# Kernel tuning notes

Hardware: AMD Instinct MI355X
Metric: run time of the kernel (lower is better)

The kernel has to match this reference:

```python
import jax, jax.numpy as jnp
import numpy as np

INPUTS, L1, L2, L3 = 40960, 256, 32, 32
B, K = 16384, 32  # batch, fixed active features per side


def setup_inputs() -> dict:
    key = jax.random.key(0)
    ks = jax.random.split(key, 12)
    wf = jax.random.randint(ks[0], (B * K,), 0, INPUTS, dtype=jnp.int64)
    bf = jax.random.randint(ks[1], (B * K,), 0, INPUTS, dtype=jnp.int64)
    offs = jnp.arange(B, dtype=jnp.int64) * K
    stm = jax.random.uniform(ks[2], (B,), dtype=jnp.float32)
    table = jax.random.normal(ks[3], (INPUTS, L1), dtype=jnp.float32) * 0.01
    ft_bias = jnp.zeros((L1,), dtype=jnp.float32)
    # xavier_uniform bounds: sqrt(6/(fan_in+fan_out))
    def xavier(k, shape):
        bound = np.sqrt(6.0 / (shape[0] + shape[1]))
        return jax.random.uniform(k, shape, jnp.float32, -bound, bound)
    W1 = xavier(ks[4], (L2, 2 * L1)); b1 = jnp.zeros((L2,), jnp.float32)
    W2 = xavier(ks[5], (L3, L2));     b2 = jnp.zeros((L3,), jnp.float32)
    Wo = xavier(ks[6], (1, L3));      bo = jnp.zeros((1,), jnp.float32)
    return {"white_features": wf, "white_offsets": offs, "black_features": bf,
            "black_offsets": offs, "stm": stm, "table": table, "ft_bias": ft_bias,
            "W1": W1, "b1": b1, "W2": W2, "b2": b2, "Wo": Wo, "bo": bo}


def _crelu(x):
    return jnp.clip(x, 0.0, 1.0)


def reference(white_features, white_offsets, black_features, black_offsets, stm,
              table, ft_bias, W1, b1, W2, b2, Wo, bo):
    nb = white_offsets.shape[0]
    # Uniform-bag EmbeddingBag(mode='sum'): gather rows and sum within each bag.
    w_acc = table[white_features.reshape(nb, -1)].sum(axis=1) + ft_bias  # [B, L1]
    b_acc = table[black_features.reshape(nb, -1)].sum(axis=1) + ft_bias  # [B, L1]
    wtm = jnp.concatenate([w_acc, b_acc], axis=1)  # [B, 2*L1]
    btm = jnp.concatenate([b_acc, w_acc], axis=1)
    s = stm.reshape(-1, 1)
    x = _crelu(s * wtm + (1.0 - s) * btm)
    x = _crelu(x @ W1.T + b1)
    x = _crelu(x @ W2.T + b2)
    return (x @ Wo.T + bo).squeeze(1)  # [B]
```

## Files before the change

kernel.cpp:

```cpp
#include <hip/hip_runtime.h>

#define KFEAT 32
#define NB 8
#define XPITCH 544
#define APITCH 272

__device__ __forceinline__ float clip01(float v) {
    return fminf(fmaxf(v, 0.0f), 1.0f);
}

__global__ __launch_bounds__(256) void quantize_table_i8(
    const float* __restrict__ src, uint* __restrict__ qt,
    float* __restrict__ scales, int nrows)
{
    const int row = blockIdx.x * 4 + (threadIdx.x >> 6);
    const int l   = threadIdx.x & 63;
    if (row >= nrows) return;

    const float4 v = reinterpret_cast<const float4*>(src)[(size_t)row * 64 + l];
    float m = fmaxf(fmaxf(fabsf(v.x), fabsf(v.y)), fmaxf(fabsf(v.z), fabsf(v.w)));
    m = fmaxf(m, __shfl_xor(m, 1));
    m = fmaxf(m, __shfl_xor(m, 2));
    m = fmaxf(m, __shfl_xor(m, 4));
    m = fmaxf(m, __shfl_xor(m, 8));
    m = fmaxf(m, __shfl_xor(m, 16));
    m = fmaxf(m, __shfl_xor(m, 32));

    const float inv = (m > 0.0f) ? 127.0f / m : 0.0f;
    const int b0 = ((int)rintf(v.x * inv)) & 0xFF;
    const int b1 = ((int)rintf(v.y * inv)) & 0xFF;
    const int b2 = ((int)rintf(v.z * inv)) & 0xFF;
    const int b3 = ((int)rintf(v.w * inv)) & 0xFF;
    qt[(size_t)row * 64 + l] = (uint)b0 | ((uint)b1 << 8) | ((uint)b2 << 16) | ((uint)b3 << 24);
    if (l == 0) scales[row] = m * (1.0f / 127.0f);
}

__global__ __launch_bounds__(256, 4) void nnue_i8_kernel(
    const int* __restrict__ wf, const int* __restrict__ bf,
    const float* __restrict__ stm, const uint* __restrict__ qt,
    const float* __restrict__ scales,
    const float* __restrict__ ft_bias,
    const float* __restrict__ W1, const float* __restrict__ b1,
    const float* __restrict__ W2, const float* __restrict__ b2,
    const float* __restrict__ Wo, const float* __restrict__ bo,
    float* __restrict__ out)
{
    __shared__ float lds[NB * XPITCH];
    __shared__ float y1s[NB][32];

    const int t   = threadIdx.x;
    const int l   = t & 63;
    const int w   = t >> 6;
    const int sub = l & 31;
    const int b0  = blockIdx.x * NB;

    {
        const int side = w & 1;
        const int eb   = w >> 1;
        const int* fp  = side ? bf : wf;

        #pragma unroll
        for (int g = 0; g < 4; ++g) {
            const int bag = g * 4 + w;
            const int iv  = fp[(size_t)(b0 + 2 * g + eb) * KFEAT + sub];

            uint v[KFEAT];
            #pragma unroll
            for (int k = 0; k < KFEAT; ++k) {
                const int row = __builtin_amdgcn_readlane(iv, k);
                v[k] = qt[(size_t)row * 64 + l];
            }

            float a0 = 0.f, a1 = 0.f, a2 = 0.f, a3 = 0.f;
            #pragma unroll
            for (int k = 0; k < KFEAT; ++k) {
                const int row  = __builtin_amdgcn_readlane(iv, k);
                const float sc = scales[row];
                const int  q   = (int)v[k];
                a0 = fmaf((float)((q << 24) >> 24), sc, a0);
                a1 = fmaf((float)((q << 16) >> 24), sc, a1);
                a2 = fmaf((float)((q <<  8) >> 24), sc, a2);
                a3 = fmaf((float)( q        >> 24), sc, a3);
            }
            *reinterpret_cast<float4*>(&lds[bag * APITCH + l * 4]) =
                make_float4(a0, a1, a2, a3);
        }
    }
    __syncthreads();

    {
        const int e = t >> 5, r = t & 31;
        const float s  = stm[b0 + e];
        const float os = 1.0f - s;
        const float4 wa0 = *reinterpret_cast<const float4*>(&lds[(2 * e + 0) * APITCH + 4 * r]);
        const float4 ba0 = *reinterpret_cast<const float4*>(&lds[(2 * e + 1) * APITCH + 4 * r]);
        const float4 wa1 = *reinterpret_cast<const float4*>(&lds[(2 * e + 0) * APITCH + 4 * (r + 32)]);
        const float4 ba1 = *reinterpret_cast<const float4*>(&lds[(2 * e + 1) * APITCH + 4 * (r + 32)]);
        const float4 fb0 = reinterpret_cast<const float4*>(ft_bias)[r];
        const float4 fb1 = reinterpret_cast<const float4*>(ft_bias)[r + 32];
        __syncthreads();

        #define MIXW(wa, ba, fb, i, hf)                                              \
        {                                                                            \
            float4 xv;                                                               \
            if (hf == 0) {                                                           \
                xv.x = clip01(fmaf(s, (wa).x, fmaf(os, (ba).x, (fb).x)));            \
                xv.y = clip01(fmaf(s, (wa).y, fmaf(os, (ba).y, (fb).y)));            \
                xv.z = clip01(fmaf(s, (wa).z, fmaf(os, (ba).z, (fb).z)));            \
                xv.w = clip01(fmaf(s, (wa).w, fmaf(os, (ba).w, (fb).w)));            \
            } else {                                                                 \
                xv.x = clip01(fmaf(s, (ba).x, fmaf(os, (wa).x, (fb).x)));            \
                xv.y = clip01(fmaf(s, (ba).y, fmaf(os, (wa).y, (fb).y)));            \
                xv.z = clip01(fmaf(s, (ba).z, fmaf(os, (wa).z, (fb).z)));            \
                xv.w = clip01(fmaf(s, (ba).w, fmaf(os, (wa).w, (fb).w)));            \
            }                                                                        \
            const int d = (hf) * 256 + 4 * (i);                                      \
            *reinterpret_cast<float4*>(&lds[e * XPITCH + (d >> 6) * 68 + (d & 63)]) = xv; \
        }
        MIXW(wa0, ba0, fb0, r,      0)
        MIXW(wa1, ba1, fb1, r + 32, 0)
        MIXW(wa0, ba0, fb0, r,      1)
        MIXW(wa1, ba1, fb1, r + 32, 1)
        #undef MIXW
    }
    __syncthreads();

    {
        const int j = t >> 3;
        const int c = t & 7;
        const float* w1p = W1 + j * 512 + c * 64;
        float acc[NB] = {0.f, 0.f, 0.f, 0.f, 0.f, 0.f, 0.f, 0.f};
        #pragma unroll
        for (int blk = 0; blk < 4; ++blk) {
            const float4 wv0 = reinterpret_cast<const float4*>(w1p + blk * 16)[0];
            const float4 wv1 = reinterpret_cast<const float4*>(w1p + blk * 16)[1];
            const float4 wv2 = reinterpret_cast<const float4*>(w1p + blk * 16)[2];
            const float4 wv3 = reinterpret_cast<const float4*>(w1p + blk * 16)[3];
            #pragma unroll
            for (int e = 0; e < NB; ++e) {
                const float* xp = &lds[e * XPITCH + c * 68 + blk * 16];
                const float4 x0 = *reinterpret_cast<const float4*>(xp + 0);
                const float4 x1 = *reinterpret_cast<const float4*>(xp + 4);
                const float4 x2 = *reinterpret_cast<const float4*>(xp + 8);
                const float4 x3 = *reinterpret_cast<const float4*>(xp + 12);
                float a = acc[e];
                a = fmaf(wv0.x, x0.x, a); a = fmaf(wv0.y, x0.y, a);
                a = fmaf(wv0.z, x0.z, a); a = fmaf(wv0.w, x0.w, a);
                a = fmaf(wv1.x, x1.x, a); a = fmaf(wv1.y, x1.y, a);
                a = fmaf(wv1.z, x1.z, a); a = fmaf(wv1.w, x1.w, a);
                a = fmaf(wv2.x, x2.x, a); a = fmaf(wv2.y, x2.y, a);
                a = fmaf(wv2.z, x2.z, a); a = fmaf(wv2.w, x2.w, a);
                a = fmaf(wv3.x, x3.x, a); a = fmaf(wv3.y, x3.y, a);
                a = fmaf(wv3.z, x3.z, a); a = fmaf(wv3.w, x3.w, a);
                acc[e] = a;
            }
        }
        #pragma unroll
        for (int e = 0; e < NB; ++e) {
            acc[e] += __shfl_xor(acc[e], 1);
            acc[e] += __shfl_xor(acc[e], 2);
            acc[e] += __shfl_xor(acc[e], 4);
        }
        if (c == 0) {
            const float bj = b1[j];
            #pragma unroll
            for (int e = 0; e < NB; ++e)
                y1s[e][j] = clip01(acc[e] + bj);
        }
    }
    __syncthreads();

    {
        const int e = t >> 5, i = t & 31;
        const float4* w2p = reinterpret_cast<const float4*>(W2 + i * 32);
        float a2 = b2[i];
        #pragma unroll
        for (int kq = 0; kq < 8; ++kq) {
            const float4 wq = w2p[kq];
            const float4 yq = *reinterpret_cast<const float4*>(&y1s[e][kq * 4]);
            a2 = fmaf(wq.x, yq.x, a2); a2 = fmaf(wq.y, yq.y, a2);
            a2 = fmaf(wq.z, yq.z, a2); a2 = fmaf(wq.w, yq.w, a2);
        }
        a2 = clip01(a2);
        float p = a2 * Wo[i];
        p += __shfl_xor(p, 1);  p += __shfl_xor(p, 2);
        p += __shfl_xor(p, 4);  p += __shfl_xor(p, 8);
        p += __shfl_xor(p, 16);
        if (i == 0) out[b0 + e] = p + bo[0];
    }
}

__global__ __launch_bounds__(256, 6) void nnue_fused_kernel(
    const int* __restrict__ wf, const int* __restrict__ bf,
    const float* __restrict__ stm, const float* __restrict__ table,
    const float* __restrict__ ft_bias,
    const float* __restrict__ W1, const float* __restrict__ b1,
    const float* __restrict__ W2, const float* __restrict__ b2,
    const float* __restrict__ Wo, const float* __restrict__ bo,
    float* __restrict__ out)
{
    __shared__ float4 accs[4][64];
    __shared__ float  xs[2 * 4 * 132];
    __shared__ float  y1s[2][32];

    const int t    = threadIdx.x;
    const int l    = t & 63;
    const int w    = t >> 6;
    const int side = w & 1;
    const int esub = w >> 1;

    const float4 ftb4 = reinterpret_cast<const float4*>(ft_bias)[l];
    const int*   fptr = side ? bf : wf;

    const int j = t >> 3;
    const int c = t & 7;
    const float* w1p = W1 + j * 512 + c * 64;
    const float* x0p = &xs[(0 * 4 + (c >> 1)) * 132 + (c & 1) * 64];
    const float* x1p = &xs[(1 * 4 + (c >> 1)) * 132 + (c & 1) * 64];

    for (int it = 0; it < 8 / 2; ++it) {
        const int b0 = blockIdx.x * 8 + it * 2;

        int idxv = fptr[(size_t)(b0 + esub) * KFEAT + (l & 31)];
        float4 acc = ftb4;
        #pragma unroll
        for (int k = 0; k < KFEAT; ++k) {
            const int row = __builtin_amdgcn_readlane(idxv, k);
            const float4 v = reinterpret_cast<const float4*>(table)[(size_t)row * 64 + l];
            acc.x += v.x; acc.y += v.y; acc.z += v.z; acc.w += v.w;
        }
        accs[w][l] = acc;
        __syncthreads();

        {
            const int e  = t >> 7;
            const int hf = (t >> 6) & 1;
            const int i  = t & 63;
            const float s  = stm[b0 + e];
            const float os = 1.0f - s;
            const float4 wa = accs[e * 2 + 0][i];
            const float4 ba = accs[e * 2 + 1][i];
            float4 x;
            if (hf == 0) {
                x.x = clip01(s * wa.x + os * ba.x);
                x.y = clip01(s * wa.y + os * ba.y);
                x.z = clip01(s * wa.z + os * ba.z);
                x.w = clip01(s * wa.w + os * ba.w);
            } else {
                x.x = clip01(s * ba.x + os * wa.x);
                x.y = clip01(s * ba.y + os * wa.y);
                x.z = clip01(s * ba.z + os * wa.z);
                x.w = clip01(s * ba.w + os * wa.w);
            }
            const int slot = hf * 64 + i;
            const int g = slot >> 5, i4 = slot & 31;
            *reinterpret_cast<float4*>(&xs[(e * 4 + g) * 132 + i4 * 4]) = x;
        }
        __syncthreads();

        float a0 = 0.0f, a1 = 0.0f;
        #pragma unroll 16
        for (int ii = 0; ii < 64; ++ii) {
            const float wv = w1p[ii];
            a0 = fmaf(wv, x0p[ii], a0);
            a1 = fmaf(wv, x1p[ii], a1);
        }
        a0 += __shfl_xor(a0, 1); a0 += __shfl_xor(a0, 2); a0 += __shfl_xor(a0, 4);
        a1 += __shfl_xor(a1, 1); a1 += __shfl_xor(a1, 2); a1 += __shfl_xor(a1, 4);
        if (c == 0) {
            const float bj = b1[j];
            y1s[0][j] = clip01(a0 + bj);
            y1s[1][j] = clip01(a1 + bj);
        }
        __syncthreads();

        if (t < 64) {
            const int e = t >> 5, i = t & 31;
            float a2 = b2[i];
            #pragma unroll
            for (int k2 = 0; k2 < 32; ++k2)
                a2 = fmaf(y1s[e][k2], W2[i * 32 + k2], a2);
            a2 = clip01(a2);
            float p = a2 * Wo[i];
            p += __shfl_xor(p, 1);  p += __shfl_xor(p, 2);
            p += __shfl_xor(p, 4);  p += __shfl_xor(p, 8);
            p += __shfl_xor(p, 16);
            if (i == 0) out[b0 + e] = p + bo[0];
        }
        __syncthreads();
    }
}

extern "C" void kernel_launch(void* const* d_in, const int* in_sizes, int n_in,
                              void* d_out, int out_size, void* d_ws, size_t ws_size,
                              hipStream_t stream) {
    const int*   wf      = (const int*)  d_in[0];
    const int*   bf      = (const int*)  d_in[2];
    const float* stm     = (const float*)d_in[4];
    const float* table   = (const float*)d_in[5];
    const float* ft_bias = (const float*)d_in[6];
    const float* W1      = (const float*)d_in[7];
    const float* b1      = (const float*)d_in[8];
    const float* W2      = (const float*)d_in[9];
    const float* b2      = (const float*)d_in[10];
    const float* Wo      = (const float*)d_in[11];
    const float* bo      = (const float*)d_in[12];
    float*       out     = (float*)d_out;

    const int B = in_sizes[1];
    const int tbl_elems = in_sizes[5];
    const int nrows = tbl_elems / 256;
    const size_t qbytes = (size_t)tbl_elems;
    const size_t need = qbytes + (size_t)nrows * sizeof(float);

    if (ws_size >= need) {
        uint*  qt     = (uint*)d_ws;
        float* scales = (float*)((char*)d_ws + qbytes);
        quantize_table_i8<<<(nrows + 3) / 4, 256, 0, stream>>>(table, qt, scales, nrows);
        nnue_i8_kernel<<<B / NB, 256, 0, stream>>>(
            wf, bf, stm, qt, scales, ft_bias, W1, b1, W2, b2, Wo, bo, out);
    } else {
        nnue_fused_kernel<<<B / 8, 256, 0, stream>>>(
            wf, bf, stm, table, ft_bias, W1, b1, W2, b2, Wo, bo, out);
    }
}
```

Before: 61.79 us.

## Retile L1 matvec to 4 outputs per thread group and fuse gather loads

```diff
diff --git a/kernel.cpp b/kernel.cpp
--- a/kernel.cpp
+++ b/kernel.cpp
@@ -63,20 +63,12 @@
         for (int g = 0; g < 4; ++g) {
             const int bag = g * 4 + w;
             const int iv  = fp[(size_t)(b0 + 2 * g + eb) * KFEAT + sub];
-
-            uint v[KFEAT];
-            #pragma unroll
-            for (int k = 0; k < KFEAT; ++k) {
-                const int row = __builtin_amdgcn_readlane(iv, k);
-                v[k] = qt[(size_t)row * 64 + l];
-            }
-
             float a0 = 0.f, a1 = 0.f, a2 = 0.f, a3 = 0.f;
             #pragma unroll
             for (int k = 0; k < KFEAT; ++k) {
                 const int row  = __builtin_amdgcn_readlane(iv, k);
+                const int  q   = (int)qt[(size_t)row * 64 + l];
                 const float sc = scales[row];
-                const int  q   = (int)v[k];
                 a0 = fmaf((float)((q << 24) >> 24), sc, a0);
                 a1 = fmaf((float)((q << 16) >> 24), sc, a1);
                 a2 = fmaf((float)((q <<  8) >> 24), sc, a2);
@@ -126,46 +118,75 @@
     __syncthreads();
 
     {
-        const int j = t >> 3;
-        const int c = t & 7;
-        const float* w1p = W1 + j * 512 + c * 64;
-        float acc[NB] = {0.f, 0.f, 0.f, 0.f, 0.f, 0.f, 0.f, 0.f};
-        #pragma unroll
-        for (int blk = 0; blk < 4; ++blk) {
-            const float4 wv0 = reinterpret_cast<const float4*>(w1p + blk * 16)[0];
-            const float4 wv1 = reinterpret_cast<const float4*>(w1p + blk * 16)[1];
-            const float4 wv2 = reinterpret_cast<const float4*>(w1p + blk * 16)[2];
-            const float4 wv3 = reinterpret_cast<const float4*>(w1p + blk * 16)[3];
-            #pragma unroll
-            for (int e = 0; e < NB; ++e) {
-                const float* xp = &lds[e * XPITCH + c * 68 + blk * 16];
+        const int jg = t >> 5;
+        const int ch = t & 31;
+        const float* w1p = W1 + (4 * jg) * 512 + ch * 16;
+
+        float4 wreg[4][4];
+        #pragma unroll
+        for (int r = 0; r < 4; ++r)
+            #pragma unroll
+            for (int q = 0; q < 4; ++q)
+                wreg[r][q] = *reinterpret_cast<const float4*>(w1p + r * 512 + q * 4);
+
+        const float4 b14 = *reinterpret_cast<const float4*>(b1 + 4 * jg);
+        const int d = ch * 16;
+        const int xoff = (d >> 6) * 68 + (d & 63);
+
+        #pragma unroll
+        for (int eh = 0; eh < 2; ++eh) {
+            float acc[4][4];
+            #pragma unroll
+            for (int r = 0; r < 4; ++r)
+                #pragma unroll
+                for (int el = 0; el < 4; ++el) acc[r][el] = 0.0f;
+
+            #pragma unroll
+            for (int el = 0; el < 4; ++el) {
+                const int e = eh * 4 + el;
+                const float* xp = &lds[e * XPITCH + xoff];
                 const float4 x0 = *reinterpret_cast<const float4*>(xp + 0);
                 const float4 x1 = *reinterpret_cast<const float4*>(xp + 4);
                 const float4 x2 = *reinterpret_cast<const float4*>(xp + 8);
                 const float4 x3 = *reinterpret_cast<const float4*>(xp + 12);
-                float a = acc[e];
-                a = fmaf(wv0.x, x0.x, a); a = fmaf(wv0.y, x0.y, a);
-                a = fmaf(wv0.z, x0.z, a); a = fmaf(wv0.w, x0.w, a);
-                a = fmaf(wv1.x, x1.x, a); a = fmaf(wv1.y, x1.y, a);
-                a = fmaf(wv1.z, x1.z, a); a = fmaf(wv1.w, x1.w, a);
-                a = fmaf(wv2.x, x2.x, a); a = fmaf(wv2.y, x2.y, a);
-                a = fmaf(wv2.z, x2.z, a); a = fmaf(wv2.w, x2.w, a);
-                a = fmaf(wv3.x, x3.x, a); a = fmaf(wv3.y, x3.y, a);
-                a = fmaf(wv3.z, x3.z, a); a = fmaf(wv3.w, x3.w, a);
-                acc[e] = a;
+                #pragma unroll
+                for (int r = 0; r < 4; ++r) {
+                    float a = acc[r][el];
+                    a = fmaf(wreg[r][0].x, x0.x, a); a = fmaf(wreg[r][0].y, x0.y, a);
+                    a = fmaf(wreg[r][0].z, x0.z, a); a = fmaf(wreg[r][0].w, x0.w, a);
+                    a = fmaf(wreg[r][1].x, x1.x, a); a = fmaf(wreg[r][1].y, x1.y, a);
+                    a = fmaf(wreg[r][1].z, x1.z, a); a = fmaf(wreg[r][1].w, x1.w, a);
+                    a = fmaf(wreg[r][2].x, x2.x, a); a = fmaf(wreg[r][2].y, x2.y, a);
+                    a = fmaf(wreg[r][2].z, x2.z, a); a = fmaf(wreg[r][2].w, x2.w, a);
+                    a = fmaf(wreg[r][3].x, x3.x, a); a = fmaf(wreg[r][3].y, x3.y, a);
+                    a = fmaf(wreg[r][3].z, x3.z, a); a = fmaf(wreg[r][3].w, x3.w, a);
+                    acc[r][el] = a;
+                }
             }
-        }
-        #pragma unroll
-        for (int e = 0; e < NB; ++e) {
-            acc[e] += __shfl_xor(acc[e], 1);
-            acc[e] += __shfl_xor(acc[e], 2);
-            acc[e] += __shfl_xor(acc[e], 4);
-        }
-        if (c == 0) {
-            const float bj = b1[j];
-            #pragma unroll
-            for (int e = 0; e < NB; ++e)
-                y1s[e][j] = clip01(acc[e] + bj);
+
+            #pragma unroll
+            for (int r = 0; r < 4; ++r)
+                #pragma unroll
+                for (int el = 0; el < 4; ++el) {
+                    float a = acc[r][el];
+                    a += __shfl_xor(a, 1);  a += __shfl_xor(a, 2);
+                    a += __shfl_xor(a, 4);  a += __shfl_xor(a, 8);
+                    a += __shfl_xor(a, 16);
+                    acc[r][el] = a;
+                }
+
+            if (ch == 0) {
+                #pragma unroll
+                for (int el = 0; el < 4; ++el) {
+                    const int e = eh * 4 + el;
+                    float4 y;
+                    y.x = clip01(acc[0][el] + b14.x);
+                    y.y = clip01(acc[1][el] + b14.y);
+                    y.z = clip01(acc[2][el] + b14.z);
+                    y.w = clip01(acc[3][el] + b14.w);
+                    *reinterpret_cast<float4*>(&y1s[e][4 * jg]) = y;
+                }
+            }
         }
     }
     __syncthreads();
```

Measured after the change: 67.17 us. 8.7% more time.

## Split i8 gather and MLP into separate kernels via workspace accumulators

Applied to the files above, without the earlier changes.

```diff
diff --git a/kernel.cpp b/kernel.cpp
--- a/kernel.cpp
+++ b/kernel.cpp
@@ -35,7 +35,164 @@
     if (l == 0) scales[row] = m * (1.0f / 127.0f);
 }
 
-__global__ __launch_bounds__(256, 4) void nnue_i8_kernel(
+__global__ __launch_bounds__(256, 8) void gather_i8_kernel(
+    const int* __restrict__ wf, const int* __restrict__ bf,
+    const uint* __restrict__ qt, const float* __restrict__ scales,
+    float* __restrict__ accs)
+{
+    const int t    = threadIdx.x;
+    const int l    = t & 63;
+    const int w    = t >> 6;
+    const int sub  = l & 31;
+    const int bag  = blockIdx.x * 4 + w;
+    const int e    = bag >> 1;
+    const int side = bag & 1;
+    const int* fp  = side ? bf : wf;
+
+    const int iv = fp[(size_t)e * KFEAT + sub];
+    float a0 = 0.f, a1 = 0.f, a2 = 0.f, a3 = 0.f;
+    #pragma unroll
+    for (int k = 0; k < KFEAT; ++k) {
+        const int row  = __builtin_amdgcn_readlane(iv, k);
+        const int  q   = (int)qt[(size_t)row * 64 + l];
+        const float sc = scales[row];
+        a0 = fmaf((float)((q << 24) >> 24), sc, a0);
+        a1 = fmaf((float)((q << 16) >> 24), sc, a1);
+        a2 = fmaf((float)((q <<  8) >> 24), sc, a2);
+        a3 = fmaf((float)( q        >> 24), sc, a3);
+    }
+    *reinterpret_cast<float4*>(&accs[(size_t)bag * 256 + l * 4]) =
+        make_float4(a0, a1, a2, a3);
+}
+
+__global__ __launch_bounds__(256, 8) void mlp_kernel(
+    const float* __restrict__ accs, const float* __restrict__ stm,
+    const float* __restrict__ ft_bias,
+    const float* __restrict__ W1, const float* __restrict__ b1,
+    const float* __restrict__ W2, const float* __restrict__ b2,
+    const float* __restrict__ Wo, const float* __restrict__ bo,
+    float* __restrict__ out)
+{
+    __shared__ float lds[NB * XPITCH];
+    __shared__ float y1s[NB][32];
+
+    const int t  = threadIdx.x;
+    const int l  = t & 63;
+    const int w  = t >> 6;
+    const int b0 = blockIdx.x * NB;
+
+    #pragma unroll
+    for (int g = 0; g < 4; ++g) {
+        const int lbag = g * 4 + w;
+        const float4 v = *reinterpret_cast<const float4*>(
+            &accs[((size_t)2 * b0 + lbag) * 256 + l * 4]);
+        *reinterpret_cast<float4*>(&lds[lbag * APITCH + l * 4]) = v;
+    }
+    __syncthreads();
+
+    {
+        const int e = t >> 5, r = t & 31;
+        const float s  = stm[b0 + e];
+        const float os = 1.0f - s;
+        const float4 wa0 = *reinterpret_cast<const float4*>(&lds[(2 * e + 0) * APITCH + 4 * r]);
+        const float4 ba0 = *reinterpret_cast<const float4*>(&lds[(2 * e + 1) * APITCH + 4 * r]);
+        const float4 wa1 = *reinterpret_cast<const float4*>(&lds[(2 * e + 0) * APITCH + 4 * (r + 32)]);
+        const float4 ba1 = *reinterpret_cast<const float4*>(&lds[(2 * e + 1) * APITCH + 4 * (r + 32)]);
+        const float4 fb0 = reinterpret_cast<const float4*>(ft_bias)[r];
+        const float4 fb1 = reinterpret_cast<const float4*>(ft_bias)[r + 32];
+        __syncthreads();
+
+        #define MIXW(wa, ba, fb, i, hf)                                              \
+        {                                                                            \
+            float4 xv;                                                               \
+            if (hf == 0) {                                                           \
+                xv.x = clip01(fmaf(s, (wa).x, fmaf(os, (ba).x, (fb).x)));            \
+                xv.y = clip01(fmaf(s, (wa).y, fmaf(os, (ba).y, (fb).y)));            \
+                xv.z = clip01(fmaf(s, (wa).z, fmaf(os, (ba).z, (fb).z)));            \
+                xv.w = clip01(fmaf(s, (wa).w, fmaf(os, (ba).w, (fb).w)));            \
+            } else {                                                                 \
+                xv.x = clip01(fmaf(s, (ba).x, fmaf(os, (wa).x, (fb).x)));            \
+                xv.y = clip01(fmaf(s, (ba).y, fmaf(os, (wa).y, (fb).y)));            \
+                xv.z = clip01(fmaf(s, (ba).z, fmaf(os, (wa).z, (fb).z)));            \
+                xv.w = clip01(fmaf(s, (ba).w, fmaf(os, (wa).w, (fb).w)));            \
+            }                                                                        \
+            const int d = (hf) * 256 + 4 * (i);                                      \
+            *reinterpret_cast<float4*>(&lds[e * XPITCH + (d >> 6) * 68 + (d & 63)]) = xv; \
+        }
+        MIXW(wa0, ba0, fb0, r,      0)
+        MIXW(wa1, ba1, fb1, r + 32, 0)
+        MIXW(wa0, ba0, fb0, r,      1)
+        MIXW(wa1, ba1, fb1, r + 32, 1)
+        #undef MIXW
+    }
+    __syncthreads();
+
+    {
+        const int j = t >> 3;
+        const int c = t & 7;
+        const float* w1p = W1 + j * 512 + c * 64;
+        float acc[NB] = {0.f, 0.f, 0.f, 0.f, 0.f, 0.f, 0.f, 0.f};
+        #pragma unroll
+        for (int blk = 0; blk < 4; ++blk) {
+            const float4 wv0 = reinterpret_cast<const float4*>(w1p + blk * 16)[0];
+            const float4 wv1 = reinterpret_cast<const float4*>(w1p + blk * 16)[1];
+            const float4 wv2 = reinterpret_cast<const float4*>(w1p + blk * 16)[2];
+            const float4 wv3 = reinterpret_cast<const float4*>(w1p + blk * 16)[3];
+            #pragma unroll
+            for (int e = 0; e < NB; ++e) {
+                const float* xp = &lds[e * XPITCH + c * 68 + blk * 16];
+                const float4 x0 = *reinterpret_cast<const float4*>(xp + 0);
+                const float4 x1 = *reinterpret_cast<const float4*>(xp + 4);
+                const float4 x2 = *reinterpret_cast<const float4*>(xp + 8);
+                const float4 x3 = *reinterpret_cast<const float4*>(xp + 12);
+                float a = acc[e];
+                a = fmaf(wv0.x, x0.x, a); a = fmaf(wv0.y, x0.y, a);
+                a = fmaf(wv0.z, x0.z, a); a = fmaf(wv0.w, x0.w, a);
+                a = fmaf(wv1.x, x1.x, a); a = fmaf(wv1.y, x1.y, a);
+                a = fmaf(wv1.z, x1.z, a); a = fmaf(wv1.w, x1.w, a);
+                a = fmaf(wv2.x, x2.x, a); a = fmaf(wv2.y, x2.y, a);
+                a = fmaf(wv2.z, x2.z, a); a = fmaf(wv2.w, x2.w, a);
+                a = fmaf(wv3.x, x3.x, a); a = fmaf(wv3.y, x3.y, a);
+                a = fmaf(wv3.z, x3.z, a); a = fmaf(wv3.w, x3.w, a);
+                acc[e] = a;
+            }
+        }
+        #pragma unroll
+        for (int e = 0; e < NB; ++e) {
+            acc[e] += __shfl_xor(acc[e], 1);
+            acc[e] += __shfl_xor(acc[e], 2);
+            acc[e] += __shfl_xor(acc[e], 4);
+        }
+        if (c == 0) {
+            const float bj = b1[j];
+            #pragma unroll
+            for (int e = 0; e < NB; ++e)
+                y1s[e][j] = clip01(acc[e] + bj);
+        }
+    }
+    __syncthreads();
+
+    {
+        const int e = t >> 5, i = t & 31;
+        const float4* w2p = reinterpret_cast<const float4*>(W2 + i * 32);
+        float a2 = b2[i];
+        #pragma unroll
+        for (int kq = 0; kq < 8; ++kq) {
+            const float4 wq = w2p[kq];
+            const float4 yq = *reinterpret_cast<const float4*>(&y1s[e][kq * 4]);
+            a2 = fmaf(wq.x, yq.x, a2); a2 = fmaf(wq.y, yq.y, a2);
+            a2 = fmaf(wq.z, yq.z, a2); a2 = fmaf(wq.w, yq.w, a2);
+        }
+        a2 = clip01(a2);
+        float p = a2 * Wo[i];
+        p += __shfl_xor(p, 1);  p += __shfl_xor(p, 2);
+        p += __shfl_xor(p, 4);  p += __shfl_xor(p, 8);
+        p += __shfl_xor(p, 16);
+        if (i == 0) out[b0 + e] = p + bo[0];
+    }
+}
+
+__global__ __launch_bounds__(256, 8) void nnue_i8_fused(
     const int* __restrict__ wf, const int* __restrict__ bf,
     const float* __restrict__ stm, const uint* __restrict__ qt,
     const float* __restrict__ scales,
@@ -58,25 +215,16 @@
         const int side = w & 1;
         const int eb   = w >> 1;
         const int* fp  = side ? bf : wf;
-
         #pragma unroll
         for (int g = 0; g < 4; ++g) {
             const int bag = g * 4 + w;
             const int iv  = fp[(size_t)(b0 + 2 * g + eb) * KFEAT + sub];
-
-            uint v[KFEAT];
-            #pragma unroll
-            for (int k = 0; k < KFEAT; ++k) {
-                const int row = __builtin_amdgcn_readlane(iv, k);
-                v[k] = qt[(size_t)row * 64 + l];
-            }
-
             float a0 = 0.f, a1 = 0.f, a2 = 0.f, a3 = 0.f;
             #pragma unroll
             for (int k = 0; k < KFEAT; ++k) {
                 const int row  = __builtin_amdgcn_readlane(iv, k);
+                const int  q   = (int)qt[(size_t)row * 64 + l];
                 const float sc = scales[row];
-                const int  q   = (int)v[k];
                 a0 = fmaf((float)((q << 24) >> 24), sc, a0);
                 a1 = fmaf((float)((q << 16) >> 24), sc, a1);
                 a2 = fmaf((float)((q <<  8) >> 24), sc, a2);
@@ -310,14 +458,25 @@
     const int B = in_sizes[1];
     const int tbl_elems = in_sizes[5];
     const int nrows = tbl_elems / 256;
-    const size_t qbytes = (size_t)tbl_elems;
-    const size_t need = qbytes + (size_t)nrows * sizeof(float);
-
-    if (ws_size >= need) {
+    const size_t qbytes  = (size_t)tbl_elems;
+    const size_t sbytes  = (size_t)nrows * sizeof(float);
+    const size_t abytes  = (size_t)B * 2 * 256 * sizeof(float);
+    const size_t need_q  = qbytes + sbytes;
+    const size_t need_sp = need_q + abytes;
+
+    if (ws_size >= need_sp) {
+        uint*  qt     = (uint*)d_ws;
+        float* scales = (float*)((char*)d_ws + qbytes);
+        float* accs   = (float*)((char*)d_ws + need_q);
+        quantize_table_i8<<<(nrows + 3) / 4, 256, 0, stream>>>(table, qt, scales, nrows);
+        gather_i8_kernel<<<(B * 2) / 4, 256, 0, stream>>>(wf, bf, qt, scales, accs);
+        mlp_kernel<<<B / NB, 256, 0, stream>>>(
+            accs, stm, ft_bias, W1, b1, W2, b2, Wo, bo, out);
+    } else if (ws_size >= need_q) {
         uint*  qt     = (uint*)d_ws;
         float* scales = (float*)((char*)d_ws + qbytes);
         quantize_table_i8<<<(nrows + 3) / 4, 256, 0, stream>>>(table, qt, scales, nrows);
-        nnue_i8_kernel<<<B / NB, 256, 0, stream>>>(
+        nnue_i8_fused<<<B / NB, 256, 0, stream>>>(
             wf, bf, stm, qt, scales, ft_bias, W1, b1, W2, b2, Wo, bo, out);
     } else {
         nnue_fused_kernel<<<B / 8, 256, 0, stream>>>(
```

After: 78.49 us. 27.0% more time.
